# Performance work log

Measured on AMD Instinct MI355X. Metric: run time of the kernel, lower is better.

## Reference

```python
import jax, jax.numpy as jnp
import numpy as np

NUM_QUBITS = 512
NUM_CORES = 16
CORE_SIZE = 64
HIDDEN = 128
BATCH = 2048


def setup_inputs() -> dict:
    key = jax.random.key(0)
    k1, k2, k3 = jax.random.split(key, 3)
    last_assignment = jax.random.randint(k1, (BATCH, NUM_QUBITS), 0, NUM_CORES, dtype=jnp.int32)
    adjacency = jnp.ones((NUM_CORES, NUM_CORES), dtype=jnp.float32)  # all-to-all core graph
    qubit_embedding = jax.random.normal(k2, (NUM_QUBITS + 1, HIDDEN), dtype=jnp.float32)
    gcn_weight = jax.random.normal(k3, (HIDDEN, HIDDEN), dtype=jnp.float32) * (1.0 / np.sqrt(HIDDEN))
    gcn_bias = jnp.zeros((HIDDEN,), dtype=jnp.float32)
    return {
        'last_assignment': last_assignment,
        'adjacency': adjacency,
        'qubit_embedding': qubit_embedding,
        'gcn_weight': gcn_weight,
        'gcn_bias': gcn_bias,
    }


def reference(last_assignment, adjacency, qubit_embedding, gcn_weight, gcn_bias):
    B, Q = last_assignment.shape
    C = adjacency.shape[0]
    # --- replace the sequential per-qubit scatter loop with a single cumsum ---
    # pos[b,q] = number of earlier qubits assigned to the same core (the loop's
    # running counter idx); core index C (the extra row) always writes slot 0
    # because the loop resets its counter every iteration.
    oh = jax.nn.one_hot(last_assignment, C + 1, dtype=jnp.int32)        # [B,Q,C+1]
    cnt = jnp.cumsum(oh, axis=1)                                        # inclusive counts
    pos = jnp.take_along_axis(cnt, last_assignment[..., None], axis=2)[..., 0] - 1
    pos = jnp.where(last_assignment == C, 0, pos)
    buf = jnp.full((B, C + 1, CORE_SIZE), Q, dtype=jnp.int32)           # padding id = num_qubits
    b_idx = jnp.arange(B)[:, None]
    q_idx = jnp.broadcast_to(jnp.arange(Q, dtype=jnp.int32)[None, :], (B, Q))
    buf = buf.at[b_idx, last_assignment, pos].set(q_idx, mode='drop')
    buf = buf[:, :C, :]                                                 # drop overflow core row
    # --- embedding (padding row forced to zero, as nn.Embedding padding_idx) ---
    tbl = qubit_embedding.at[Q].set(0.0)
    qubit_embs = tbl[buf]                                               # [B,C,core_size,H]
    core_embs = qubit_embs.max(axis=2)                                  # [B,C,H]
    # --- GCNConv(add_self_loops=False): D^{-1/2} A D^{-1/2} (X W^T) + b ---
    deg = adjacency.sum(axis=0)
    dinv = jnp.where(deg > 0, 1.0 / jnp.sqrt(deg), 0.0)
    a_norm = adjacency * dinv[:, None] * dinv[None, :]                  # symmetric norm
    h = jnp.einsum('bch,oh->bco', core_embs, gcn_weight)                # lin (PyG: x @ W^T)
    out = jnp.einsum('ij,bjo->bio', a_norm, h) + gcn_bias               # [B,C,H]
    return out
```

## Files before the change

### kernel.cpp

```cpp
#include <hip/hip_runtime.h>
#include <stdint.h>

typedef unsigned short u16;
typedef unsigned int u32;
typedef unsigned long long u64;

typedef __bf16 bf16x8 __attribute__((ext_vector_type(8)));
typedef float f32x4 __attribute__((ext_vector_type(4)));
typedef u16 u16x8 __attribute__((ext_vector_type(8)));

#define NQ 512
#define NC 16
#define NH 128
#define NB 2048
#define QE_KEYS (513*128)
#define WT_OFF  QE_KEYS
#define GW_ELEMS (128*128)
#define A_OFF (WT_OFF + GW_ELEMS)
#define LSEG 1088
#define ESTC 544
#define ESEG (16*ESTC)

static __device__ __forceinline__ u16 f2bf_rne(float f){
  u32 u = __float_as_uint(f);
  u += 0x7fffu + ((u>>16)&1u);
  return (u16)(u>>16);
}
static __device__ __forceinline__ u32 pack_rne(float lo, float hi){
  return (u32)f2bf_rne(lo) | ((u32)f2bf_rne(hi)<<16);
}
static __device__ __forceinline__ u16 key_of(float f){
  u16 b = f2bf_rne(f);
  return (b & 0x8000u) ? (u16)~b : (u16)(b | 0x8000u);
}
static __device__ __forceinline__ u32 unkey2(u32 w){
  u32 s = w & 0x80008000u;
  return w ^ ~(s - (s >> 15));
}

union Frag { u32 u[4]; uint4 u4; bf16x8 f; };
union U8   { u16x8 v; int w[4]; u32 uw[4]; uint4 u4; u16 h[8]; };

__global__ void prepass_kernel(const float* __restrict__ qe,
                               const float* __restrict__ gw,
                               const float* __restrict__ adj,
                               u16* __restrict__ ws)
{
  if (blockIdx.x == 0) {
    __shared__ float sD[16];
    int t = threadIdx.x;
    if (t < 16) {
      float s = 0.f;
      for (int i = 0; i < 16; ++i) s += adj[i*16 + t];
      sD[t] = (s > 0.f) ? (1.0f / sqrtf(s)) : 0.f;
    }
    __syncthreads();
    int i = t >> 4, jp = (t & 15) * 2;
    float lo = (jp   < 16) ? adj[i*16 + jp]   * sD[i] * sD[jp]   : 0.f;
    float hi = (jp+1 < 16) ? adj[i*16 + jp+1] * sD[i] * sD[jp+1] : 0.f;
    ((u32*)(ws + A_OFF))[t] = pack_rne(lo, hi);
    return;
  }
  int idx = (blockIdx.x - 1) * 256 + threadIdx.x;
  if (idx < QE_KEYS/8) {
    int i8 = idx * 8;
    uint4 o;
    if (i8 >= 512*NH) {
      o.x = 0x80008000u; o.y = 0x80008000u; o.z = 0x80008000u; o.w = 0x80008000u;
    } else {
      const float4* p = (const float4*)(qe + i8);
      float4 a = p[0], b = p[1];
      o.x = (u32)key_of(a.x) | ((u32)key_of(a.y)<<16);
      o.y = (u32)key_of(a.z) | ((u32)key_of(a.w)<<16);
      o.z = (u32)key_of(b.x) | ((u32)key_of(b.y)<<16);
      o.w = (u32)key_of(b.z) | ((u32)key_of(b.w)<<16);
    }
    *(uint4*)(ws + i8) = o;
  } else if (idx < QE_KEYS/8 + GW_ELEMS/8) {
    int j8 = (idx - QE_KEYS/8) * 8;
    const float4* p = (const float4*)(gw + j8);
    float4 a = p[0], b = p[1];
    uint4 o;
    o.x = pack_rne(a.x, a.y); o.y = pack_rne(a.z, a.w);
    o.z = pack_rne(b.x, b.y); o.w = pack_rne(b.z, b.w);
    *(uint4*)(ws + WT_OFF + j8) = o;
  }
}

__global__ __launch_bounds__(256, 4)
void core_snapshot_kernel(const int* __restrict__ la,
                          const u16* __restrict__ ws,
                          const float* __restrict__ gb,
                          float* __restrict__ outp)
{
  __shared__ __align__(16) u16 sListAll[2*LSEG];
  __shared__ __align__(16) u16 sEAll[2*ESEG];
  __shared__ int sCnt[2][2][16];

  const int tid  = threadIdx.x;
  const int lane = tid & 63;
  const int wv   = tid >> 6;
  const int it   = wv >> 1;
  const int tw   = wv & 1;
  const int m    = lane & 15;
  const int quad = lane >> 4;
  const int item = blockIdx.x*2 + it;
  u16* sList = sListAll + it*LSEG;
  u16* sE    = sEAll    + it*ESEG;
  const u16* qt = ws;
  const u16* wt = ws + WT_OFF;

  {
    uint4 f = make_uint4(0x02000200u,0x02000200u,0x02000200u,0x02000200u);
    *(uint4*)&sList[tw*512 + lane*8] = f;
  }
  __syncthreads();

  int av[4];
  #pragma unroll
  for (int ch = 0; ch < 4; ++ch) av[ch] = la[item*NQ + (tw*4 + ch)*64 + lane];
  const u64 lmask = (1ull << lane) - 1ull;
  u32 runbase = 0;
  u32 rankrel[4];
  #pragma unroll
  for (int ch = 0; ch < 4; ++ch) {
    u32 cnt = 0, intra = 0;
    #pragma unroll
    for (int c = 0; c < 16; ++c) {
      u64 mk = __ballot(av[ch] == c);
      if (lane == c)    cnt   = (u32)__popcll(mk);
      if (av[ch] == c)  intra = (u32)__popcll(mk & lmask);
    }
    u32 base = (u32)__shfl((int)runbase, av[ch]);
    rankrel[ch] = base + intra;
    runbase += cnt;
  }
  if (lane < 16) sCnt[it][tw][lane] = (int)runbase;
  if (tw == 0) {
    #pragma unroll
    for (int ch = 0; ch < 4; ++ch) {
      u32 rank = rankrel[ch];
      if (rank < 64) sList[av[ch]*64 + (rank&3)*16 + (rank>>2)] = (u16)(ch*64 + lane);
    }
  }
  __syncthreads();
  u32 cntv;
  if (tw == 1) {
    #pragma unroll
    for (int ch = 0; ch < 4; ++ch) {
      u32 rank = (u32)sCnt[it][0][av[ch]] + rankrel[ch];
      if (rank < 64) sList[av[ch]*64 + (rank&3)*16 + (rank>>2)] = (u16)((4 + ch)*64 + lane);
    }
    cntv = runbase + (u32)((lane < 16) ? sCnt[it][0][lane] : 0);
  } else {
    cntv = runbase + (u32)((lane < 16) ? sCnt[it][1][lane] : 0);
  }
  __syncthreads();

  const u16* qb = qt + m*8;
  #pragma unroll 1
  for (int pp = 0; pp < 4; ++pp) {
    const int c0 = tw*8 + pp*2, c1 = c0 + 1;
    const int cnt0 = __shfl((int)cntv, c0);
    const int cnt1 = __shfl((int)cntv, c1);
    U8 S0a, S1a, S0b, S1b;
    S0a.u4 = *(const uint4*)&sList[c0*64 + quad*16];
    S1a.u4 = *(const uint4*)&sList[c0*64 + quad*16 + 8];
    S0b.u4 = *(const uint4*)&sList[c1*64 + quad*16];
    S1b.u4 = *(const uint4*)&sList[c1*64 + quad*16 + 8];
    U8 Ta[8], Tb[8];
    #pragma unroll
    for (int k = 0; k < 8; ++k) Ta[k].u4 = *(const uint4*)(qb + (int)S0a.h[k]*NH);
    #pragma unroll
    for (int k = 0; k < 8; ++k) Tb[k].u4 = *(const uint4*)(qb + (int)S0b.h[k]*NH);

    U8 A; A.v = (u16x8)0;
    #pragma unroll
    for (int k = 0; k < 8; ++k) A.v = __builtin_elementwise_max(A.v, Ta[k].v);
    if (cnt0 > 32) {
      U8 T[4];
      #pragma unroll
      for (int k = 0; k < 4; ++k) T[k].u4 = *(const uint4*)(qb + (int)S1a.h[k]*NH);
      #pragma unroll
      for (int k = 0; k < 4; ++k) A.v = __builtin_elementwise_max(A.v, T[k].v);
    }
    if (cnt0 > 48) {
      U8 T[4];
      #pragma unroll
      for (int k = 0; k < 4; ++k) T[k].u4 = *(const uint4*)(qb + (int)S1a.h[4+k]*NH);
      #pragma unroll
      for (int k = 0; k < 4; ++k) A.v = __builtin_elementwise_max(A.v, T[k].v);
    }
    if (cnt0 < 64) { U8 Z; Z.v = (u16x8)(u16)0x8000u; A.v = __builtin_elementwise_max(A.v, Z.v); }
    *(uint4*)&sE[c0*ESTC + quad*136 + m*8] = A.u4;

    U8 B; B.v = (u16x8)0;
    #pragma unroll
    for (int k = 0; k < 8; ++k) B.v = __builtin_elementwise_max(B.v, Tb[k].v);
    if (cnt1 > 32) {
      U8 T[4];
      #pragma unroll
      for (int k = 0; k < 4; ++k) T[k].u4 = *(const uint4*)(qb + (int)S1b.h[k]*NH);
      #pragma unroll
      for (int k = 0; k < 4; ++k) B.v = __builtin_elementwise_max(B.v, T[k].v);
    }
    if (cnt1 > 48) {
      U8 T[4];
      #pragma unroll
      for (int k = 0; k < 4; ++k) T[k].u4 = *(const uint4*)(qb + (int)S1b.h[4+k]*NH);
      #pragma unroll
      for (int k = 0; k < 4; ++k) B.v = __builtin_elementwise_max(B.v, T[k].v);
    }
    if (cnt1 < 64) { U8 Z; Z.v = (u16x8)(u16)0x8000u; B.v = __builtin_elementwise_max(B.v, Z.v); }
    *(uint4*)&sE[c1*ESTC + quad*136 + m*8] = B.u4;
  }
  __syncthreads();

  bf16x8 af[4];
  #pragma unroll
  for (int ks = 0; ks < 4; ++ks) {
    const u16* pb = &sE[m*ESTC + ks*32 + quad*8];
    U8 P0, P1, P2, P3;
    P0.u4 = *(const uint4*)(pb);
    P1.u4 = *(const uint4*)(pb + 136);
    P2.u4 = *(const uint4*)(pb + 272);
    P3.u4 = *(const uint4*)(pb + 408);
    P0.v = __builtin_elementwise_max(P0.v, P1.v);
    P2.v = __builtin_elementwise_max(P2.v, P3.v);
    P0.v = __builtin_elementwise_max(P0.v, P2.v);
    Frag f;
    #pragma unroll
    for (int j = 0; j < 4; ++j) f.u[j] = unkey2(P0.uw[j]);
    af[ks] = f.f;
  }
  Frag anf;
  anf.u4 = *(const uint4*)(ws + A_OFF + m*32 + quad*8);

  #pragma unroll
  for (int tt = 0; tt < 4; ++tt) {
    int t = tw*4 + tt;
    f32x4 acc = {0.f, 0.f, 0.f, 0.f};
    #pragma unroll
    for (int ks = 0; ks < 4; ++ks) {
      bf16x8 bfr = *(const bf16x8*)(wt + (t*16 + m)*NH + ks*32 + quad*8);
      acc = __builtin_amdgcn_mfma_f32_16x16x32_bf16(af[ks], bfr, acc, 0, 0, 0);
    }
    float d16[4], d32[4], lo[4], hi[4];
    #pragma unroll
    for (int r = 0; r < 4; ++r) {
      d16[r] = __shfl_down(acc[r], 16);
      d32[r] = __shfl_down(acc[r], 32);
    }
    #pragma unroll
    for (int r = 0; r < 4; ++r) {
      lo[r] = (quad == 0) ? acc[r] : d16[r];
      hi[r] = (quad == 0) ? d16[r] : d32[r];
    }
    Frag hb;
    hb.u[0] = pack_rne(lo[0], lo[1]); hb.u[1] = pack_rne(lo[2], lo[3]);
    hb.u[2] = pack_rne(hi[0], hi[1]); hb.u[3] = pack_rne(hi[2], hi[3]);
    if (quad >= 2) { hb.u[0]=0; hb.u[1]=0; hb.u[2]=0; hb.u[3]=0; }
    float biasv = gb[t*16 + m];
    f32x4 o4 = {biasv, biasv, biasv, biasv};
    o4 = __builtin_amdgcn_mfma_f32_16x16x32_bf16(anf.f, hb.f, o4, 0, 0, 0);
    float* op = outp + item*(NC*NH) + t*16 + m;
    #pragma unroll
    for (int r = 0; r < 4; ++r) op[(quad*4 + r)*NH] = o4[r];
  }
}

extern "C" void kernel_launch(void* const* d_in, const int* in_sizes, int n_in,
                              void* d_out, int out_size, void* d_ws, size_t ws_size,
                              hipStream_t stream) {
  const int*   la  = (const int*)d_in[0];
  const float* adj = (const float*)d_in[1];
  const float* qe  = (const float*)d_in[2];
  const float* gw  = (const float*)d_in[3];
  const float* gb  = (const float*)d_in[4];
  float* outp = (float*)d_out;
  u16* ws = (u16*)d_ws;

  int pre_blocks = 1 + (QE_KEYS/8 + GW_ELEMS/8 + 255)/256;
  prepass_kernel<<<pre_blocks, 256, 0, stream>>>(qe, gw, adj, ws);
  core_snapshot_kernel<<<NB/2, 256, 0, stream>>>(la, ws, gb, outp);
}
```

Baseline: 89.05 us.

## Stage embedding key table in LDS and process eight items per 1024-thread block

Each 1024-thread block copies the whole bf16 embedding key table (~128KB) into shared memory and serves the per-core gathers from LDS instead of global/L2. Four wave-teams each handle one batch item per round over two rounds, so the table load is amortized over eight items. The per-quad max reduction now uses cross-lane shuffles instead of a shared-memory partial pass. The cost is a large per-block table copy and heavy LDS use that limits blocks per CU, with only 256 blocks launched.

```diff
diff --git a/kernel.cpp b/kernel.cpp
--- a/kernel.cpp
+++ b/kernel.cpp
@@ -17,9 +17,16 @@
 #define WT_OFF  QE_KEYS
 #define GW_ELEMS (128*128)
 #define A_OFF (WT_OFF + GW_ELEMS)
+
 #define LSEG 1088
-#define ESTC 544
-#define ESEG (16*ESTC)
+#define ESTRIDE 136
+#define ESEG 2176
+
+#define TBL_BYTES 131328
+#define LIST_OFF_B TBL_BYTES
+#define E_OFF_B    (LIST_OFF_B + 4*2*LSEG)
+#define CNT_OFF_B  (E_OFF_B + 4*2*ESEG)
+#define SMEM_BYTES (CNT_OFF_B + 4*64*4)
 
 static __device__ __forceinline__ u16 f2bf_rne(float f){
   u32 u = __float_as_uint(f);
@@ -87,185 +94,199 @@
   }
 }
 
-__global__ __launch_bounds__(256, 4)
+__global__ __launch_bounds__(1024, 4)
 void core_snapshot_kernel(const int* __restrict__ la,
                           const u16* __restrict__ ws,
                           const float* __restrict__ gb,
                           float* __restrict__ outp)
 {
-  __shared__ __align__(16) u16 sListAll[2*LSEG];
-  __shared__ __align__(16) u16 sEAll[2*ESEG];
-  __shared__ int sCnt[2][2][16];
+  extern __shared__ __align__(16) unsigned char smem[];
+  u16* sTable = (u16*)smem;
 
   const int tid  = threadIdx.x;
   const int lane = tid & 63;
-  const int wv   = tid >> 6;
-  const int it   = wv >> 1;
-  const int tw   = wv & 1;
+  const int wvg  = tid >> 6;
+  const int team = wvg >> 2;
+  const int w    = wvg & 3;
   const int m    = lane & 15;
   const int quad = lane >> 4;
-  const int item = blockIdx.x*2 + it;
-  u16* sList = sListAll + it*LSEG;
-  u16* sE    = sEAll    + it*ESEG;
-  const u16* qt = ws;
+  const int ttid = w*64 + lane;
+
+  u16* sList = (u16*)(smem + LIST_OFF_B) + team*LSEG;
+  u16* sE    = (u16*)(smem + E_OFF_B)    + team*ESEG;
+  int* sCnt  = (int*)(smem + CNT_OFF_B)  + team*64;
+
+  {
+    const uint4* g = (const uint4*)ws;
+    uint4* d = (uint4*)smem;
+    #pragma unroll
+    for (int i = 0; i < 8; ++i) d[i*1024 + tid] = g[i*1024 + tid];
+    if (tid < 16) d[8192 + tid] = g[8192 + tid];
+  }
+
   const u16* wt = ws + WT_OFF;
-
-  {
-    uint4 f = make_uint4(0x02000200u,0x02000200u,0x02000200u,0x02000200u);
-    *(uint4*)&sList[tw*512 + lane*8] = f;
-  }
-  __syncthreads();
-
-  int av[4];
-  #pragma unroll
-  for (int ch = 0; ch < 4; ++ch) av[ch] = la[item*NQ + (tw*4 + ch)*64 + lane];
-  const u64 lmask = (1ull << lane) - 1ull;
-  u32 runbase = 0;
-  u32 rankrel[4];
-  #pragma unroll
-  for (int ch = 0; ch < 4; ++ch) {
-    u32 cnt = 0, intra = 0;
-    #pragma unroll
-    for (int c = 0; c < 16; ++c) {
-      u64 mk = __ballot(av[ch] == c);
-      if (lane == c)    cnt   = (u32)__popcll(mk);
-      if (av[ch] == c)  intra = (u32)__popcll(mk & lmask);
-    }
-    u32 base = (u32)__shfl((int)runbase, av[ch]);
-    rankrel[ch] = base + intra;
-    runbase += cnt;
-  }
-  if (lane < 16) sCnt[it][tw][lane] = (int)runbase;
-  if (tw == 0) {
-    #pragma unroll
-    for (int ch = 0; ch < 4; ++ch) {
-      u32 rank = rankrel[ch];
-      if (rank < 64) sList[av[ch]*64 + (rank&3)*16 + (rank>>2)] = (u16)(ch*64 + lane);
-    }
-  }
-  __syncthreads();
-  u32 cntv;
-  if (tw == 1) {
-    #pragma unroll
-    for (int ch = 0; ch < 4; ++ch) {
-      u32 rank = (u32)sCnt[it][0][av[ch]] + rankrel[ch];
-      if (rank < 64) sList[av[ch]*64 + (rank&3)*16 + (rank>>2)] = (u16)((4 + ch)*64 + lane);
-    }
-    cntv = runbase + (u32)((lane < 16) ? sCnt[it][0][lane] : 0);
-  } else {
-    cntv = runbase + (u32)((lane < 16) ? sCnt[it][1][lane] : 0);
-  }
-  __syncthreads();
-
-  const u16* qb = qt + m*8;
-  #pragma unroll 1
-  for (int pp = 0; pp < 4; ++pp) {
-    const int c0 = tw*8 + pp*2, c1 = c0 + 1;
-    const int cnt0 = __shfl((int)cntv, c0);
-    const int cnt1 = __shfl((int)cntv, c1);
-    U8 S0a, S1a, S0b, S1b;
-    S0a.u4 = *(const uint4*)&sList[c0*64 + quad*16];
-    S1a.u4 = *(const uint4*)&sList[c0*64 + quad*16 + 8];
-    S0b.u4 = *(const uint4*)&sList[c1*64 + quad*16];
-    S1b.u4 = *(const uint4*)&sList[c1*64 + quad*16 + 8];
-    U8 Ta[8], Tb[8];
-    #pragma unroll
-    for (int k = 0; k < 8; ++k) Ta[k].u4 = *(const uint4*)(qb + (int)S0a.h[k]*NH);
-    #pragma unroll
-    for (int k = 0; k < 8; ++k) Tb[k].u4 = *(const uint4*)(qb + (int)S0b.h[k]*NH);
-
-    U8 A; A.v = (u16x8)0;
-    #pragma unroll
-    for (int k = 0; k < 8; ++k) A.v = __builtin_elementwise_max(A.v, Ta[k].v);
-    if (cnt0 > 32) {
-      U8 T[4];
-      #pragma unroll
-      for (int k = 0; k < 4; ++k) T[k].u4 = *(const uint4*)(qb + (int)S1a.h[k]*NH);
-      #pragma unroll
-      for (int k = 0; k < 4; ++k) A.v = __builtin_elementwise_max(A.v, T[k].v);
-    }
-    if (cnt0 > 48) {
-      U8 T[4];
-      #pragma unroll
-      for (int k = 0; k < 4; ++k) T[k].u4 = *(const uint4*)(qb + (int)S1a.h[4+k]*NH);
-      #pragma unroll
-      for (int k = 0; k < 4; ++k) A.v = __builtin_elementwise_max(A.v, T[k].v);
-    }
-    if (cnt0 < 64) { U8 Z; Z.v = (u16x8)(u16)0x8000u; A.v = __builtin_elementwise_max(A.v, Z.v); }
-    *(uint4*)&sE[c0*ESTC + quad*136 + m*8] = A.u4;
-
-    U8 B; B.v = (u16x8)0;
-    #pragma unroll
-    for (int k = 0; k < 8; ++k) B.v = __builtin_elementwise_max(B.v, Tb[k].v);
-    if (cnt1 > 32) {
-      U8 T[4];
-      #pragma unroll
-      for (int k = 0; k < 4; ++k) T[k].u4 = *(const uint4*)(qb + (int)S1b.h[k]*NH);
-      #pragma unroll
-      for (int k = 0; k < 4; ++k) B.v = __builtin_elementwise_max(B.v, T[k].v);
-    }
-    if (cnt1 > 48) {
-      U8 T[4];
-      #pragma unroll
-      for (int k = 0; k < 4; ++k) T[k].u4 = *(const uint4*)(qb + (int)S1b.h[4+k]*NH);
-      #pragma unroll
-      for (int k = 0; k < 4; ++k) B.v = __builtin_elementwise_max(B.v, T[k].v);
-    }
-    if (cnt1 < 64) { U8 Z; Z.v = (u16x8)(u16)0x8000u; B.v = __builtin_elementwise_max(B.v, Z.v); }
-    *(uint4*)&sE[c1*ESTC + quad*136 + m*8] = B.u4;
-  }
-  __syncthreads();
-
-  bf16x8 af[4];
-  #pragma unroll
-  for (int ks = 0; ks < 4; ++ks) {
-    const u16* pb = &sE[m*ESTC + ks*32 + quad*8];
-    U8 P0, P1, P2, P3;
-    P0.u4 = *(const uint4*)(pb);
-    P1.u4 = *(const uint4*)(pb + 136);
-    P2.u4 = *(const uint4*)(pb + 272);
-    P3.u4 = *(const uint4*)(pb + 408);
-    P0.v = __builtin_elementwise_max(P0.v, P1.v);
-    P2.v = __builtin_elementwise_max(P2.v, P3.v);
-    P0.v = __builtin_elementwise_max(P0.v, P2.v);
-    Frag f;
-    #pragma unroll
-    for (int j = 0; j < 4; ++j) f.u[j] = unkey2(P0.uw[j]);
-    af[ks] = f.f;
-  }
   Frag anf;
   anf.u4 = *(const uint4*)(ws + A_OFF + m*32 + quad*8);
-
-  #pragma unroll
-  for (int tt = 0; tt < 4; ++tt) {
-    int t = tw*4 + tt;
-    f32x4 acc = {0.f, 0.f, 0.f, 0.f};
-    #pragma unroll
-    for (int ks = 0; ks < 4; ++ks) {
-      bf16x8 bfr = *(const bf16x8*)(wt + (t*16 + m)*NH + ks*32 + quad*8);
-      acc = __builtin_amdgcn_mfma_f32_16x16x32_bf16(af[ks], bfr, acc, 0, 0, 0);
-    }
-    float d16[4], d32[4], lo[4], hi[4];
-    #pragma unroll
-    for (int r = 0; r < 4; ++r) {
-      d16[r] = __shfl_down(acc[r], 16);
-      d32[r] = __shfl_down(acc[r], 32);
-    }
-    #pragma unroll
-    for (int r = 0; r < 4; ++r) {
-      lo[r] = (quad == 0) ? acc[r] : d16[r];
-      hi[r] = (quad == 0) ? d16[r] : d32[r];
-    }
-    Frag hb;
-    hb.u[0] = pack_rne(lo[0], lo[1]); hb.u[1] = pack_rne(lo[2], lo[3]);
-    hb.u[2] = pack_rne(hi[0], hi[1]); hb.u[3] = pack_rne(hi[2], hi[3]);
-    if (quad >= 2) { hb.u[0]=0; hb.u[1]=0; hb.u[2]=0; hb.u[3]=0; }
-    float biasv = gb[t*16 + m];
-    f32x4 o4 = {biasv, biasv, biasv, biasv};
-    o4 = __builtin_amdgcn_mfma_f32_16x16x32_bf16(anf.f, hb.f, o4, 0, 0, 0);
-    float* op = outp + item*(NC*NH) + t*16 + m;
-    #pragma unroll
-    for (int r = 0; r < 4; ++r) op[(quad*4 + r)*NH] = o4[r];
+  const u64 lmask = (1ull << lane) - 1ull;
+
+  for (int rnd = 0; rnd < 2; ++rnd) {
+    const int item = blockIdx.x*8 + rnd*4 + team;
+
+    if (ttid < 128) {
+      uint4 f = make_uint4(0x02000200u,0x02000200u,0x02000200u,0x02000200u);
+      *(uint4*)&sList[ttid*8] = f;
+    }
+
+    int av[2];
+    av[0] = la[item*NQ + (w*2 + 0)*64 + lane];
+    av[1] = la[item*NQ + (w*2 + 1)*64 + lane];
+    u32 runbase = 0;
+    u32 rankrel[2];
+    #pragma unroll
+    for (int ch = 0; ch < 2; ++ch) {
+      u32 cnt = 0, intra = 0;
+      #pragma unroll
+      for (int c = 0; c < 16; ++c) {
+        u64 mk = __ballot(av[ch] == c);
+        if (lane == c)    cnt   = (u32)__popcll(mk);
+        if (av[ch] == c)  intra = (u32)__popcll(mk & lmask);
+      }
+      u32 base = (u32)__shfl((int)runbase, av[ch]);
+      rankrel[ch] = base + intra;
+      runbase += cnt;
+    }
+    if (lane < 16) sCnt[w*16 + lane] = (int)runbase;
+    __syncthreads();
+
+    u32 basew = 0, cntv = 0;
+    if (lane < 16) {
+      int c0 = sCnt[ 0 + lane], c1 = sCnt[16 + lane];
+      int c2 = sCnt[32 + lane], c3 = sCnt[48 + lane];
+      cntv  = (u32)(c0 + c1 + c2 + c3);
+      basew = (w > 0 ? (u32)c0 : 0u) + (w > 1 ? (u32)c1 : 0u)
+            + (w > 2 ? (u32)c2 : 0u);
+    }
+    #pragma unroll
+    for (int ch = 0; ch < 2; ++ch) {
+      u32 rank = (u32)__shfl((int)basew, av[ch]) + rankrel[ch];
+      if (rank < 64)
+        sList[av[ch]*64 + (rank&3)*16 + (rank>>2)] = (u16)((w*2 + ch)*64 + lane);
+    }
+    __syncthreads();
+
+    const u16* qb = sTable + m*8;
+    #pragma unroll 1
+    for (int pp = 0; pp < 2; ++pp) {
+      const int c0 = w*4 + pp*2, c1 = c0 + 1;
+      const int cnt0 = __shfl((int)cntv, c0);
+      const int cnt1 = __shfl((int)cntv, c1);
+      U8 S0a, S1a, S0b, S1b;
+      S0a.u4 = *(const uint4*)&sList[c0*64 + quad*16];
+      S1a.u4 = *(const uint4*)&sList[c0*64 + quad*16 + 8];
+      S0b.u4 = *(const uint4*)&sList[c1*64 + quad*16];
+      S1b.u4 = *(const uint4*)&sList[c1*64 + quad*16 + 8];
+      U8 Ta[8], Tb[8];
+      #pragma unroll
+      for (int k = 0; k < 8; ++k) Ta[k].u4 = *(const uint4*)(qb + (int)S0a.h[k]*NH);
+      #pragma unroll
+      for (int k = 0; k < 8; ++k) Tb[k].u4 = *(const uint4*)(qb + (int)S0b.h[k]*NH);
+
+      U8 A; A.v = (u16x8)0;
+      #pragma unroll
+      for (int k = 0; k < 8; ++k) A.v = __builtin_elementwise_max(A.v, Ta[k].v);
+      if (cnt0 > 32) {
+        U8 T[4];
+        #pragma unroll
+        for (int k = 0; k < 4; ++k) T[k].u4 = *(const uint4*)(qb + (int)S1a.h[k]*NH);
+        #pragma unroll
+        for (int k = 0; k < 4; ++k) A.v = __builtin_elementwise_max(A.v, T[k].v);
+      }
+      if (cnt0 > 48) {
+        U8 T[4];
+        #pragma unroll
+        for (int k = 0; k < 4; ++k) T[k].u4 = *(const uint4*)(qb + (int)S1a.h[4+k]*NH);
+        #pragma unroll
+        for (int k = 0; k < 4; ++k) A.v = __builtin_elementwise_max(A.v, T[k].v);
+      }
+      if (cnt0 < 64) { U8 Z; Z.v = (u16x8)(u16)0x8000u; A.v = __builtin_elementwise_max(A.v, Z.v); }
+
+      U8 B; B.v = (u16x8)0;
+      #pragma unroll
+      for (int k = 0; k < 8; ++k) B.v = __builtin_elementwise_max(B.v, Tb[k].v);
+      if (cnt1 > 32) {
+        U8 T[4];
+        #pragma unroll
+        for (int k = 0; k < 4; ++k) T[k].u4 = *(const uint4*)(qb + (int)S1b.h[k]*NH);
+        #pragma unroll
+        for (int k = 0; k < 4; ++k) B.v = __builtin_elementwise_max(B.v, T[k].v);
+      }
+      if (cnt1 > 48) {
+        U8 T[4];
+        #pragma unroll
+        for (int k = 0; k < 4; ++k) T[k].u4 = *(const uint4*)(qb + (int)S1b.h[4+k]*NH);
+        #pragma unroll
+        for (int k = 0; k < 4; ++k) B.v = __builtin_elementwise_max(B.v, T[k].v);
+      }
+      if (cnt1 < 64) { U8 Z; Z.v = (u16x8)(u16)0x8000u; B.v = __builtin_elementwise_max(B.v, Z.v); }
+
+      U8 RA, RB;
+      #pragma unroll
+      for (int j = 0; j < 4; ++j) { RA.w[j] = __shfl_xor(A.w[j], 16); RB.w[j] = __shfl_xor(B.w[j], 16); }
+      A.v = __builtin_elementwise_max(A.v, RA.v);
+      B.v = __builtin_elementwise_max(B.v, RB.v);
+      #pragma unroll
+      for (int j = 0; j < 4; ++j) { RA.w[j] = __shfl_xor(A.w[j], 32); RB.w[j] = __shfl_xor(B.w[j], 32); }
+      A.v = __builtin_elementwise_max(A.v, RA.v);
+      B.v = __builtin_elementwise_max(B.v, RB.v);
+
+      if (quad == 0) {
+        uint4 e;
+        e.x = unkey2(A.uw[0]); e.y = unkey2(A.uw[1]);
+        e.z = unkey2(A.uw[2]); e.w = unkey2(A.uw[3]);
+        *(uint4*)&sE[c0*ESTRIDE + m*8] = e;
+        e.x = unkey2(B.uw[0]); e.y = unkey2(B.uw[1]);
+        e.z = unkey2(B.uw[2]); e.w = unkey2(B.uw[3]);
+        *(uint4*)&sE[c1*ESTRIDE + m*8] = e;
+      }
+    }
+    __syncthreads();
+
+    bf16x8 af[4];
+    #pragma unroll
+    for (int ks = 0; ks < 4; ++ks)
+      af[ks] = *(const bf16x8*)&sE[m*ESTRIDE + ks*32 + quad*8];
+
+    #pragma unroll
+    for (int tt = 0; tt < 2; ++tt) {
+      int t = w*2 + tt;
+      f32x4 acc = {0.f, 0.f, 0.f, 0.f};
+      #pragma unroll
+      for (int ks = 0; ks < 4; ++ks) {
+        bf16x8 bfr = *(const bf16x8*)(wt + (t*16 + m)*NH + ks*32 + quad*8);
+        acc = __builtin_amdgcn_mfma_f32_16x16x32_bf16(af[ks], bfr, acc, 0, 0, 0);
+      }
+      float d16[4], d32[4], lo[4], hi[4];
+      #pragma unroll
+      for (int r = 0; r < 4; ++r) {
+        d16[r] = __shfl_down(acc[r], 16);
+        d32[r] = __shfl_down(acc[r], 32);
+      }
+      #pragma unroll
+      for (int r = 0; r < 4; ++r) {
+        lo[r] = (quad == 0) ? acc[r] : d16[r];
+        hi[r] = (quad == 0) ? d16[r] : d32[r];
+      }
+      Frag hb;
+      hb.u[0] = pack_rne(lo[0], lo[1]); hb.u[1] = pack_rne(lo[2], lo[3]);
+      hb.u[2] = pack_rne(hi[0], hi[1]); hb.u[3] = pack_rne(hi[2], hi[3]);
+      if (quad >= 2) { hb.u[0]=0; hb.u[1]=0; hb.u[2]=0; hb.u[3]=0; }
+      float biasv = gb[t*16 + m];
+      f32x4 o4 = {biasv, biasv, biasv, biasv};
+      o4 = __builtin_amdgcn_mfma_f32_16x16x32_bf16(anf.f, hb.f, o4, 0, 0, 0);
+      float* op = outp + item*(NC*NH) + t*16 + m;
+      #pragma unroll
+      for (int r = 0; r < 4; ++r) op[(quad*4 + r)*NH] = o4[r];
+    }
   }
 }
 
@@ -280,7 +301,15 @@
   float* outp = (float*)d_out;
   u16* ws = (u16*)d_ws;
 
+  static bool s_attr = false;
+  if (!s_attr) {
+    (void)hipFuncSetAttribute(reinterpret_cast<const void*>(core_snapshot_kernel),
+                              hipFuncAttributeMaxDynamicSharedMemorySize,
+                              SMEM_BYTES);
+    s_attr = true;
+  }
+
   int pre_blocks = 1 + (QE_KEYS/8 + GW_ELEMS/8 + 255)/256;
   prepass_kernel<<<pre_blocks, 256, 0, stream>>>(qe, gw, adj, ws);
-  core_snapshot_kernel<<<NB/2, 256, 0, stream>>>(la, ws, gb, outp);
-}
+  core_snapshot_kernel<<<NB/8, 1024, SMEM_BYTES, stream>>>(la, ws, gb, outp);
+}
```

After: 103.0 us. +15.7%, slower.

## Process one batch item per block with four waves sharing the work

Applied to the files above, without the earlier changes.

Restructures the kernel so each 256-thread block handles a single batch item, with all four waves cooperating on ranking, scatter, max-pooling and the MFMA output tiles, instead of two items per block at two waves each. The grid doubles to NB blocks, per-block shared memory halves, and launch bounds now target 8 blocks per CU. The goal is shorter per-wave serial work and more resident blocks for better latency hiding. The cost is a four-way cross-wave prefix over counts and each wave doing less work per item.

```diff
diff --git a/kernel.cpp b/kernel.cpp
--- a/kernel.cpp
+++ b/kernel.cpp
@@ -17,9 +17,9 @@
 #define WT_OFF  QE_KEYS
 #define GW_ELEMS (128*128)
 #define A_OFF (WT_OFF + GW_ELEMS)
+
 #define LSEG 1088
 #define ESTC 544
-#define ESEG (16*ESTC)
 
 static __device__ __forceinline__ u16 f2bf_rne(float f){
   u32 u = __float_as_uint(f);
@@ -87,43 +87,38 @@
   }
 }
 
-__global__ __launch_bounds__(256, 4)
+__global__ __launch_bounds__(256, 8)
 void core_snapshot_kernel(const int* __restrict__ la,
                           const u16* __restrict__ ws,
                           const float* __restrict__ gb,
                           float* __restrict__ outp)
 {
-  __shared__ __align__(16) u16 sListAll[2*LSEG];
-  __shared__ __align__(16) u16 sEAll[2*ESEG];
-  __shared__ int sCnt[2][2][16];
+  __shared__ __align__(16) u16 sList[LSEG];
+  __shared__ __align__(16) u16 sE[16*ESTC];
+  __shared__ int sCnt[64];
 
   const int tid  = threadIdx.x;
   const int lane = tid & 63;
-  const int wv   = tid >> 6;
-  const int it   = wv >> 1;
-  const int tw   = wv & 1;
+  const int w    = tid >> 6;
   const int m    = lane & 15;
   const int quad = lane >> 4;
-  const int item = blockIdx.x*2 + it;
-  u16* sList = sListAll + it*LSEG;
-  u16* sE    = sEAll    + it*ESEG;
+  const int item = blockIdx.x;
   const u16* qt = ws;
   const u16* wt = ws + WT_OFF;
 
-  {
+  if (tid < 128) {
     uint4 f = make_uint4(0x02000200u,0x02000200u,0x02000200u,0x02000200u);
-    *(uint4*)&sList[tw*512 + lane*8] = f;
-  }
-  __syncthreads();
-
-  int av[4];
-  #pragma unroll
-  for (int ch = 0; ch < 4; ++ch) av[ch] = la[item*NQ + (tw*4 + ch)*64 + lane];
+    *(uint4*)&sList[tid*8] = f;
+  }
+
+  int av[2];
+  av[0] = la[item*NQ + (w*2 + 0)*64 + lane];
+  av[1] = la[item*NQ + (w*2 + 1)*64 + lane];
   const u64 lmask = (1ull << lane) - 1ull;
   u32 runbase = 0;
-  u32 rankrel[4];
-  #pragma unroll
-  for (int ch = 0; ch < 4; ++ch) {
+  u32 rankrel[2];
+  #pragma unroll
+  for (int ch = 0; ch < 2; ++ch) {
     u32 cnt = 0, intra = 0;
     #pragma unroll
     for (int c = 0; c < 16; ++c) {
@@ -135,32 +130,29 @@
     rankrel[ch] = base + intra;
     runbase += cnt;
   }
-  if (lane < 16) sCnt[it][tw][lane] = (int)runbase;
-  if (tw == 0) {
-    #pragma unroll
-    for (int ch = 0; ch < 4; ++ch) {
-      u32 rank = rankrel[ch];
-      if (rank < 64) sList[av[ch]*64 + (rank&3)*16 + (rank>>2)] = (u16)(ch*64 + lane);
-    }
-  }
+  if (lane < 16) sCnt[w*16 + lane] = (int)runbase;
   __syncthreads();
-  u32 cntv;
-  if (tw == 1) {
-    #pragma unroll
-    for (int ch = 0; ch < 4; ++ch) {
-      u32 rank = (u32)sCnt[it][0][av[ch]] + rankrel[ch];
-      if (rank < 64) sList[av[ch]*64 + (rank&3)*16 + (rank>>2)] = (u16)((4 + ch)*64 + lane);
-    }
-    cntv = runbase + (u32)((lane < 16) ? sCnt[it][0][lane] : 0);
-  } else {
-    cntv = runbase + (u32)((lane < 16) ? sCnt[it][1][lane] : 0);
+
+  u32 basew = 0, cntv = 0;
+  if (lane < 16) {
+    int c0 = sCnt[ 0 + lane], c1 = sCnt[16 + lane];
+    int c2 = sCnt[32 + lane], c3 = sCnt[48 + lane];
+    cntv  = (u32)(c0 + c1 + c2 + c3);
+    basew = (w > 0 ? (u32)c0 : 0u) + (w > 1 ? (u32)c1 : 0u)
+          + (w > 2 ? (u32)c2 : 0u);
+  }
+  #pragma unroll
+  for (int ch = 0; ch < 2; ++ch) {
+    u32 rank = (u32)__shfl((int)basew, av[ch]) + rankrel[ch];
+    if (rank < 64)
+      sList[av[ch]*64 + (rank&3)*16 + (rank>>2)] = (u16)((w*2 + ch)*64 + lane);
   }
   __syncthreads();
 
   const u16* qb = qt + m*8;
   #pragma unroll 1
-  for (int pp = 0; pp < 4; ++pp) {
-    const int c0 = tw*8 + pp*2, c1 = c0 + 1;
+  for (int pp = 0; pp < 2; ++pp) {
+    const int c0 = w*4 + pp*2, c1 = c0 + 1;
     const int cnt0 = __shfl((int)cntv, c0);
     const int cnt1 = __shfl((int)cntv, c1);
     U8 S0a, S1a, S0b, S1b;
@@ -237,8 +229,8 @@
   anf.u4 = *(const uint4*)(ws + A_OFF + m*32 + quad*8);
 
   #pragma unroll
-  for (int tt = 0; tt < 4; ++tt) {
-    int t = tw*4 + tt;
+  for (int tt = 0; tt < 2; ++tt) {
+    int t = w*2 + tt;
     f32x4 acc = {0.f, 0.f, 0.f, 0.f};
     #pragma unroll
     for (int ks = 0; ks < 4; ++ks) {
@@ -282,5 +274,5 @@
 
   int pre_blocks = 1 + (QE_KEYS/8 + GW_ELEMS/8 + 255)/256;
   prepass_kernel<<<pre_blocks, 256, 0, stream>>>(qe, gw, adj, ws);
-  core_snapshot_kernel<<<NB/2, 256, 0, stream>>>(la, ws, gb, outp);
-}
+  core_snapshot_kernel<<<NB, 256, 0, stream>>>(la, ws, gb, outp);
+}
```

New measurement: 97.50 us. 1.09x slower.
